# Performance work log

Measured on AMD Instinct MI355X. Metric: run time of the kernel, lower is better.

## Reference

```python
import jax, jax.numpy as jnp
import numpy as np

DIM = 2048
STATE = 16
BATCH = 2
SEQ = 2048
LN_EPS = 1e-5


def setup_inputs() -> dict:
    key = jax.random.key(0)
    ks = jax.random.split(key, 12)
    d, n = DIM, STATE
    inp = {
        "x": jax.random.normal(ks[0], (BATCH, SEQ, d), dtype=jnp.float32),
        "ln_gamma": jnp.ones((d,), dtype=jnp.float32),
        "ln_beta": jnp.zeros((d,), dtype=jnp.float32),
        # proj_in: Linear(d, 2d) (spectral-normed; weights treated as effective)
        "W_in": jax.random.normal(ks[1], (2 * d, d), dtype=jnp.float32) / np.sqrt(d),
        "b_in": jnp.zeros((2 * d,), dtype=jnp.float32),
        "state_A": jax.random.normal(ks[2], (n, d), dtype=jnp.float32) * 0.01,
        "W_B": jax.random.normal(ks[3], (n, d), dtype=jnp.float32) / np.sqrt(d),
        "b_B": jnp.zeros((n,), dtype=jnp.float32),
        "W_C": jax.random.normal(ks[4], (n, d), dtype=jnp.float32) / np.sqrt(d),
        "b_C": jnp.zeros((n,), dtype=jnp.float32),
        "W_dt": jax.random.normal(ks[5], (d, d), dtype=jnp.float32) / np.sqrt(d),
        "b_dt": jnp.zeros((d,), dtype=jnp.float32),
        "W_out": jax.random.normal(ks[6], (d, d), dtype=jnp.float32) / np.sqrt(d),
        "b_out": jnp.zeros((d,), dtype=jnp.float32),
    }
    return inp


def reference(x, ln_gamma, ln_beta, W_in, b_in, state_A, W_B, b_B, W_C, b_C,
              W_dt, b_dt, W_out, b_out):
    residual = x
    # LayerNorm over last dim
    mu = jnp.mean(x, axis=-1, keepdims=True)
    var = jnp.mean(jnp.square(x - mu), axis=-1, keepdims=True)
    xn = (x - mu) * jax.lax.rsqrt(var + LN_EPS) * ln_gamma + ln_beta
    # input projection and gate split
    xz = jnp.einsum('bsd,ed->bse', xn, W_in) + b_in          # (B,S,2D)
    x_ssm, z = jnp.split(xz, 2, axis=-1)                      # (B,S,D) each
    # dt = clamp(softplus(proj_dt(x_ssm)), max=1.0)
    dt = jnp.minimum(jax.nn.softplus(jnp.einsum('bsd,ed->bse', x_ssm, W_dt) + b_dt), 1.0)
    Bm = jnp.einsum('bsd,nd->bsn', x_ssm, W_B) + b_B          # (B,S,N)
    Cm = jnp.einsum('bsd,nd->bsn', x_ssm, W_C) + b_C          # (B,S,N)
    # A_bar[b,s,n,d] = exp(state_A[n,d] * dt[b,s,d])
    A_bar = jnp.exp(state_A[None, None, :, :] * dt[:, :, None, :])  # (B,S,N,D)
    # y[b,s,d] = sum_n C[b,s,n]*B[b,s,n]*A_bar[b,s,n,d] * x_ssm[b,s,d]
    y = jnp.einsum('bsn,bsnd->bsd', Cm * Bm, A_bar) * x_ssm
    gated = y * jax.nn.silu(z)
    out = jnp.einsum('bsd,ed->bse', gated, W_out) + b_out
    return out + residual
```

## Files before the change

### kernel.cpp

```cpp
#include <hip/hip_runtime.h>

typedef unsigned short u16;
typedef float f32x4 __attribute__((ext_vector_type(4)));
typedef __bf16 bf16x8 __attribute__((ext_vector_type(8)));

__device__ __forceinline__ u16 f2bf(float f) {
    unsigned u = __float_as_uint(f);
    u += 0x7FFFu + ((u >> 16) & 1u);
    return (u16)(u >> 16);
}
__device__ __forceinline__ float b2f(u16 h) {
    return __uint_as_float(((unsigned)h) << 16);
}

__device__ __forceinline__ void async16(const u16* g, u16* l) {
    __builtin_amdgcn_global_load_lds(
        (__attribute__((address_space(1))) void*)(u16*)g,
        (__attribute__((address_space(3))) void*)l,
        16, 0, 0);
}

#define T_TOK 4096
#define DIM   2048

__global__ __launch_bounds__(256) void castln_kernel(const float* __restrict__ W_in,
                                                     u16* __restrict__ wb_in,
                                                     const float* __restrict__ x,
                                                     const float* __restrict__ g,
                                                     const float* __restrict__ b,
                                                     u16* __restrict__ o) {
    __shared__ float s1[4], s2[4];
    int blk = blockIdx.x, tid = threadIdx.x;
    if (blk < 8192) {
        int i = blk * 256 + tid;
        float4 f = ((const float4*)W_in)[i];
        ushort4 u;
        u.x = f2bf(f.x); u.y = f2bf(f.y); u.z = f2bf(f.z); u.w = f2bf(f.w);
        ((ushort4*)wb_in)[i] = u;
        return;
    }
    int t = blk - 8192;
    int wave = tid >> 6, lane = tid & 63;
    size_t base = (size_t)t * DIM;
    int d0 = tid * 8;
    float4 v0 = *(const float4*)(x + base + d0);
    float4 v1 = *(const float4*)(x + base + d0 + 4);
    float v[8] = {v0.x, v0.y, v0.z, v0.w, v1.x, v1.y, v1.z, v1.w};
    float s = 0.f;
#pragma unroll
    for (int j = 0; j < 8; ++j) s += v[j];
#pragma unroll
    for (int o2 = 32; o2; o2 >>= 1) s += __shfl_xor(s, o2);
    if (lane == 0) s1[wave] = s;
    __syncthreads();
    float mu = (s1[0] + s1[1] + s1[2] + s1[3]) * (1.f / DIM);
    float q = 0.f;
#pragma unroll
    for (int j = 0; j < 8; ++j) { float dd = v[j] - mu; q += dd * dd; }
#pragma unroll
    for (int o2 = 32; o2; o2 >>= 1) q += __shfl_xor(q, o2);
    if (lane == 0) s2[wave] = q;
    __syncthreads();
    float var = (s2[0] + s2[1] + s2[2] + s2[3]) * (1.f / DIM);
    float rs = rsqrtf(var + 1e-5f);
    float4 g0 = *(const float4*)(g + d0), g1 = *(const float4*)(g + d0 + 4);
    float4 b0 = *(const float4*)(b + d0), b1 = *(const float4*)(b + d0 + 4);
    float gv[8] = {g0.x, g0.y, g0.z, g0.w, g1.x, g1.y, g1.z, g1.w};
    float bv[8] = {b0.x, b0.y, b0.z, b0.w, b1.x, b1.y, b1.z, b1.w};
    ushort4 r0, r1;
    u16* rp0 = (u16*)&r0; u16* rp1 = (u16*)&r1;
#pragma unroll
    for (int j = 0; j < 4; ++j) {
        rp0[j] = f2bf((v[j] - mu) * rs * gv[j] + bv[j]);
        rp1[j] = f2bf((v[j + 4] - mu) * rs * gv[j + 4] + bv[j + 4]);
    }
    *(ushort4*)(o + base + d0) = r0;
    *(ushort4*)(o + base + d0 + 4) = r1;
}

__global__ __launch_bounds__(256) void cast4_kernel(const float* __restrict__ s0, u16* __restrict__ d0, int n0,
                                                    const float* __restrict__ s1, u16* __restrict__ d1, int n1,
                                                    const float* __restrict__ s2, u16* __restrict__ d2, int n2,
                                                    const float* __restrict__ s3, u16* __restrict__ d3, int n3) {
    int j = blockIdx.x * 256 + threadIdx.x;
    const float* s; u16* d;
    if (j < n0) { s = s0; d = d0; }
    else {
        j -= n0;
        if (j < n1) { s = s1; d = d1; }
        else {
            j -= n1;
            if (j < n2) { s = s2; d = d2; }
            else { j -= n2; if (j >= n3) return; s = s3; d = d3; }
        }
    }
    float4 f = ((const float4*)s)[j];
    ushort4 u;
    u.x = f2bf(f.x); u.y = f2bf(f.y); u.z = f2bf(f.z); u.w = f2bf(f.w);
    ((ushort4*)d)[j] = u;
}

#define WBM 128
#define WBN 128
#define WBK 64

__global__ __launch_bounds__(256) void gemm_wide(const u16* __restrict__ A,
                                                 const u16* __restrict__ W,
                                                 const float* __restrict__ bias,
                                                 u16* __restrict__ Xs,
                                                 u16* __restrict__ Z, int K) {
    __shared__ __align__(16) u16 lAB[(WBM + WBN) * WBK];
    const int tid = threadIdx.x;
    const int wave = tid >> 6, lane = tid & 63;
    const int quad = lane >> 4, l16 = lane & 15;
    const int tM = blockIdx.x * WBM;
    const int tN = blockIdx.y * WBN;
    const int wr = wave >> 1, wc = wave & 1;

    const int rowin = tid >> 3;
    const int col8 = ((tid & 7) ^ (rowin & 7)) * 8;
    const u16* gptr[8];
    u16* ldst[8];
#pragma unroll
    for (int i = 0; i < 8; ++i) {
        int trow = i * 32 + rowin;
        const u16* src = (i < 4) ? (A + (size_t)(tM + trow) * 2048)
                                 : (W + (size_t)(tN + (trow - WBM)) * 2048);
        gptr[i] = src + col8;
        ldst[i] = &lAB[(i * 32 + wave * 8) * WBK];
    }

    int a_off[2][4], b_off[2][4];
#pragma unroll
    for (int h = 0; h < 2; ++h) {
#pragma unroll
        for (int mi = 0; mi < 4; ++mi)
            a_off[h][mi] = (wr * 64 + mi * 16 + l16) * WBK +
                           (((h * 4 + quad) ^ (l16 & 7)) * 8);
#pragma unroll
        for (int ni = 0; ni < 4; ++ni)
            b_off[h][ni] = (WBM + wc * 64 + ni * 16 + l16) * WBK +
                           (((h * 4 + quad) ^ (l16 & 7)) * 8);
    }

    f32x4 acc[4][4] = {};

    for (int kt = 0; kt < K; kt += WBK) {
#pragma unroll
        for (int i = 0; i < 8; ++i) async16(gptr[i] + kt, ldst[i]);
        __syncthreads();
#pragma unroll
        for (int h = 0; h < 2; ++h) {
            bf16x8 af[4], bfr[4];
#pragma unroll
            for (int i = 0; i < 4; ++i) af[i] = *(const bf16x8*)&lAB[a_off[h][i]];
#pragma unroll
            for (int i = 0; i < 4; ++i) bfr[i] = *(const bf16x8*)&lAB[b_off[h][i]];
#pragma unroll
            for (int mi = 0; mi < 4; ++mi)
#pragma unroll
                for (int ni = 0; ni < 4; ++ni)
                    acc[mi][ni] = __builtin_amdgcn_mfma_f32_16x16x32_bf16(
                        af[mi], bfr[ni], acc[mi][ni], 0, 0, 0);
        }
        __syncthreads();
    }

    const bool isb_z = (tN >= 2048);
    u16* dst = isb_z ? Z : Xs;
#pragma unroll
    for (int mi = 0; mi < 4; ++mi) {
#pragma unroll
        for (int ni = 0; ni < 4; ++ni) {
            int col = tN + wc * 64 + ni * 16 + l16;
            float bv = bias[col];
            int ocol = isb_z ? (col - 2048) : col;
#pragma unroll
            for (int r = 0; r < 4; ++r) {
                int row = tM + wr * 64 + mi * 16 + quad * 4 + r;
                dst[(size_t)row * 2048 + ocol] = f2bf(acc[mi][ni][r] + bv);
            }
        }
    }
}

#define NBM 128
#define NBN 64
#define NBK 64

template <int EPI>
__global__ __launch_bounds__(256) void gemm_nw(const u16* __restrict__ A, int lda,
                                               const u16* __restrict__ W, int ldw,
                                               const float* __restrict__ bias,
                                               const float* __restrict__ resid,
                                               void* __restrict__ C, int ldc, int K,
                                               u16* __restrict__ dots) {
    __shared__ __align__(16) u16 lAB[(NBM + NBN) * NBK];
    const int tid = threadIdx.x;
    const int wave = tid >> 6, lane = tid & 63;
    const int quad = lane >> 4, l16 = lane & 15;
    const int tM = blockIdx.x * NBM;
    const int tN = blockIdx.y * NBN;
    const int wr = wave >> 1, wc = wave & 1;

    const int rowin = tid >> 3;
    const int r3 = rowin & 7;
    const int col8 = ((tid & 7) ^ r3) * 8;
    const u16* gptr[6];
    u16* ldst[6];
#pragma unroll
    for (int i = 0; i < 6; ++i) {
        int trow = i * 32 + rowin;
        const u16* src = (i < 4) ? (A + (size_t)(tM + trow) * lda)
                                 : (W + (size_t)(tN + (trow - NBM)) * ldw);
        gptr[i] = src + col8;
        ldst[i] = &lAB[(i * 32 + wave * 8) * NBK];
    }

    int a_off[2][4], b_off[2][2];
#pragma unroll
    for (int h = 0; h < 2; ++h) {
#pragma unroll
        for (int mi = 0; mi < 4; ++mi)
            a_off[h][mi] = (wr * 64 + mi * 16 + l16) * NBK +
                           (((h * 4 + quad) ^ (l16 & 7)) * 8);
#pragma unroll
        for (int ni = 0; ni < 2; ++ni)
            b_off[h][ni] = (NBM + wc * 32 + ni * 16 + l16) * NBK +
                           (((h * 4 + quad) ^ (l16 & 7)) * 8);
    }

    f32x4 acc[4][2] = {};

    for (int kt = 0; kt < K; kt += NBK) {
#pragma unroll
        for (int i = 0; i < 6; ++i) async16(gptr[i] + kt, ldst[i]);
        __syncthreads();
        bf16x8 af[2][4], bfr[2][2];
#pragma unroll
        for (int h = 0; h < 2; ++h) {
#pragma unroll
            for (int mi = 0; mi < 4; ++mi) af[h][mi] = *(const bf16x8*)&lAB[a_off[h][mi]];
#pragma unroll
            for (int ni = 0; ni < 2; ++ni) bfr[h][ni] = *(const bf16x8*)&lAB[b_off[h][ni]];
        }
#pragma unroll
        for (int h = 0; h < 2; ++h)
#pragma unroll
            for (int mi = 0; mi < 4; ++mi)
#pragma unroll
                for (int ni = 0; ni < 2; ++ni)
                    acc[mi][ni] = __builtin_amdgcn_mfma_f32_16x16x32_bf16(
                        af[h][mi], bfr[h][ni], acc[mi][ni], 0, 0, 0);
        __syncthreads();
    }

#pragma unroll
    for (int mi = 0; mi < 4; ++mi) {
#pragma unroll
        for (int ni = 0; ni < 2; ++ni) {
            int col = tN + wc * 32 + ni * 16 + l16;
            float bv = (EPI == 1 && col >= 2048) ? 0.f : bias[col];
#pragma unroll
            for (int r = 0; r < 4; ++r) {
                int row = tM + wr * 64 + mi * 16 + quad * 4 + r;
                float v = acc[mi][ni][r] + bv;
                if constexpr (EPI == 1) {
                    if (col < 2048) {
                        float sp = (v > 20.f) ? v : log1pf(__expf(v));
                        ((u16*)C)[(size_t)row * ldc + col] = f2bf(fminf(sp, 1.0f));
                    } else if (col < 2080) {
                        dots[(size_t)row * 32 + (col - 2048)] = f2bf(v);
                    }
                } else {
                    size_t idx = (size_t)row * ldc + col;
                    ((float*)C)[idx] = v + resid[idx];
                }
            }
        }
    }
}

__global__ __launch_bounds__(256) void ssm_gate_kernel(const u16* __restrict__ dtb,
                                                       const u16* __restrict__ xsb,
                                                       const u16* __restrict__ zb,
                                                       const float* __restrict__ A,
                                                       const u16* __restrict__ dots,
                                                       const float* __restrict__ bB,
                                                       const float* __restrict__ bC,
                                                       u16* __restrict__ gated) {
    __shared__ float Pl[16];
    int t = blockIdx.x, tid = threadIdx.x;
    if (tid < 16) {
        float Bv = b2f(dots[(size_t)t * 32 + tid]) + bB[tid];
        float Cv = b2f(dots[(size_t)t * 32 + 16 + tid]) + bC[tid];
        Pl[tid] = Bv * Cv;
    }
    __syncthreads();
    size_t dbase = (size_t)t * DIM;
    int d0 = tid * 8;
    ushort4 dth[2], xsh[2], zh[2];
    dth[0] = *(const ushort4*)(dtb + dbase + d0);
    dth[1] = *(const ushort4*)(dtb + dbase + d0 + 4);
    xsh[0] = *(const ushort4*)(xsb + dbase + d0);
    xsh[1] = *(const ushort4*)(xsb + dbase + d0 + 4);
    zh[0]  = *(const ushort4*)(zb + dbase + d0);
    zh[1]  = *(const ushort4*)(zb + dbase + d0 + 4);
    float dtv[8], xsv[8], zv[8];
#pragma unroll
    for (int h = 0; h < 2; ++h) {
        const u16* dp = (const u16*)&dth[h];
        const u16* xp = (const u16*)&xsh[h];
        const u16* zp = (const u16*)&zh[h];
#pragma unroll
        for (int j = 0; j < 4; ++j) {
            dtv[h * 4 + j] = b2f(dp[j]);
            xsv[h * 4 + j] = b2f(xp[j]);
            zv[h * 4 + j]  = b2f(zp[j]);
        }
    }
    float s[8] = {};
#pragma unroll
    for (int n = 0; n < 16; ++n) {
        float4 a0 = *(const float4*)(A + n * DIM + d0);
        float4 a1 = *(const float4*)(A + n * DIM + d0 + 4);
        float pn = Pl[n];
        float av[8] = {a0.x, a0.y, a0.z, a0.w, a1.x, a1.y, a1.z, a1.w};
#pragma unroll
        for (int j = 0; j < 8; ++j) s[j] += pn * __expf(av[j] * dtv[j]);
    }
    ushort4 r0, r1;
    u16* rp0 = (u16*)&r0; u16* rp1 = (u16*)&r1;
#pragma unroll
    for (int j = 0; j < 8; ++j) {
        float y = s[j] * xsv[j];
        float sz = zv[j] * (1.0f / (1.0f + __expf(-zv[j])));
        u16 hv = f2bf(y * sz);
        if (j < 4) rp0[j] = hv; else rp1[j - 4] = hv;
    }
    *(ushort4*)(gated + dbase + d0) = r0;
    *(ushort4*)(gated + dbase + d0 + 4) = r1;
}

extern "C" void kernel_launch(void* const* d_in, const int* in_sizes, int n_in,
                              void* d_out, int out_size, void* d_ws, size_t ws_size,
                              hipStream_t stream) {
    const float* x      = (const float*)d_in[0];
    const float* ln_g   = (const float*)d_in[1];
    const float* ln_b   = (const float*)d_in[2];
    const float* W_in   = (const float*)d_in[3];
    const float* b_in   = (const float*)d_in[4];
    const float* stateA = (const float*)d_in[5];
    const float* W_B    = (const float*)d_in[6];
    const float* b_B    = (const float*)d_in[7];
    const float* W_C    = (const float*)d_in[8];
    const float* b_C    = (const float*)d_in[9];
    const float* W_dt   = (const float*)d_in[10];
    const float* b_dt   = (const float*)d_in[11];
    const float* W_out  = (const float*)d_in[12];
    const float* b_out  = (const float*)d_in[13];

    char* ws = (char*)d_ws;
    u16*   wb_in  = (u16*)(ws);
    u16*   wb_out = (u16*)(ws);
    u16*   xnb    = (u16*)(ws + 16777216);
    u16*   wb_dt  = (u16*)(ws + 16777216);
    u16*   gated  = (u16*)(ws + 16777216);
    u16*   xsb    = (u16*)(ws + 33554432);
    u16*   zb     = (u16*)(ws + 50331648);
    u16*   dtb    = (u16*)(ws + 67108864);
    u16*   dotsb  = (u16*)(ws + 83886080);

    castln_kernel<<<12288, 256, 0, stream>>>(W_in, wb_in, x, ln_g, ln_b, xnb);
    gemm_wide<<<dim3(32, 32), 256, 0, stream>>>(xnb, wb_in, b_in, xsb, zb, 2048);
    cast4_kernel<<<8256, 256, 0, stream>>>(
        W_dt, wb_dt, 1048576,
        W_B,  wb_dt + (size_t)2048 * 2048, 8192,
        W_C,  wb_dt + (size_t)2064 * 2048, 8192,
        W_out, wb_out, 1048576);
    gemm_nw<1><<<dim3(32, 33), 256, 0, stream>>>(xsb, 2048, wb_dt, 2048, b_dt,
                                                 nullptr, dtb, 2048, 2048, dotsb);
    ssm_gate_kernel<<<T_TOK, 256, 0, stream>>>(dtb, xsb, zb, stateA, dotsb,
                                               b_B, b_C, gated);
    gemm_nw<2><<<dim3(32, 32), 256, 0, stream>>>(gated, 2048, wb_out, 2048, b_out,
                                                 x, (float*)d_out, 2048, 2048, nullptr);
}
```

Baseline: 394.9 us.

## Use FP8 for dt projection and fold B/C projections into input GEMM

```diff
diff --git a/kernel.cpp b/kernel.cpp
--- a/kernel.cpp
+++ b/kernel.cpp
@@ -1,6 +1,8 @@
 #include <hip/hip_runtime.h>
 
 typedef unsigned short u16;
+typedef unsigned char u8;
+typedef unsigned int u32;
 typedef float f32x4 __attribute__((ext_vector_type(4)));
 typedef __bf16 bf16x8 __attribute__((ext_vector_type(8)));
 
@@ -13,9 +15,9 @@
     return __uint_as_float(((unsigned)h) << 16);
 }
 
-__device__ __forceinline__ void async16(const u16* g, u16* l) {
+__device__ __forceinline__ void async16(const void* g, void* l) {
     __builtin_amdgcn_global_load_lds(
-        (__attribute__((address_space(1))) void*)(u16*)g,
+        (__attribute__((address_space(1))) void*)g,
         (__attribute__((address_space(3))) void*)l,
         16, 0, 0);
 }
@@ -28,9 +30,16 @@
                                                      const float* __restrict__ x,
                                                      const float* __restrict__ g,
                                                      const float* __restrict__ b,
-                                                     u16* __restrict__ o) {
+                                                     u16* __restrict__ xnb,
+                                                     const float* __restrict__ W_B,
+                                                     const float* __restrict__ W_C,
+                                                     const float* __restrict__ b_in,
+                                                     const float* __restrict__ b_B,
+                                                     const float* __restrict__ b_C,
+                                                     float* __restrict__ be) {
     __shared__ float s1[4], s2[4];
     int blk = blockIdx.x, tid = threadIdx.x;
+    int wave = tid >> 6, lane = tid & 63;
     if (blk < 8192) {
         int i = blk * 256 + tid;
         float4 f = ((const float4*)W_in)[i];
@@ -39,65 +48,109 @@
         ((ushort4*)wb_in)[i] = u;
         return;
     }
-    int t = blk - 8192;
-    int wave = tid >> 6, lane = tid & 63;
-    size_t base = (size_t)t * DIM;
-    int d0 = tid * 8;
-    float4 v0 = *(const float4*)(x + base + d0);
-    float4 v1 = *(const float4*)(x + base + d0 + 4);
-    float v[8] = {v0.x, v0.y, v0.z, v0.w, v1.x, v1.y, v1.z, v1.w};
-    float s = 0.f;
-#pragma unroll
-    for (int j = 0; j < 8; ++j) s += v[j];
-#pragma unroll
-    for (int o2 = 32; o2; o2 >>= 1) s += __shfl_xor(s, o2);
-    if (lane == 0) s1[wave] = s;
-    __syncthreads();
-    float mu = (s1[0] + s1[1] + s1[2] + s1[3]) * (1.f / DIM);
-    float q = 0.f;
-#pragma unroll
-    for (int j = 0; j < 8; ++j) { float dd = v[j] - mu; q += dd * dd; }
-#pragma unroll
-    for (int o2 = 32; o2; o2 >>= 1) q += __shfl_xor(q, o2);
-    if (lane == 0) s2[wave] = q;
-    __syncthreads();
-    float var = (s2[0] + s2[1] + s2[2] + s2[3]) * (1.f / DIM);
-    float rs = rsqrtf(var + 1e-5f);
-    float4 g0 = *(const float4*)(g + d0), g1 = *(const float4*)(g + d0 + 4);
-    float4 b0 = *(const float4*)(b + d0), b1 = *(const float4*)(b + d0 + 4);
-    float gv[8] = {g0.x, g0.y, g0.z, g0.w, g1.x, g1.y, g1.z, g1.w};
-    float bv[8] = {b0.x, b0.y, b0.z, b0.w, b1.x, b1.y, b1.z, b1.w};
-    ushort4 r0, r1;
-    u16* rp0 = (u16*)&r0; u16* rp1 = (u16*)&r1;
-#pragma unroll
-    for (int j = 0; j < 4; ++j) {
-        rp0[j] = f2bf((v[j] - mu) * rs * gv[j] + bv[j]);
-        rp1[j] = f2bf((v[j + 4] - mu) * rs * gv[j + 4] + bv[j + 4]);
-    }
-    *(ushort4*)(o + base + d0) = r0;
-    *(ushort4*)(o + base + d0 + 4) = r1;
-}
-
-__global__ __launch_bounds__(256) void cast4_kernel(const float* __restrict__ s0, u16* __restrict__ d0, int n0,
-                                                    const float* __restrict__ s1, u16* __restrict__ d1, int n1,
-                                                    const float* __restrict__ s2, u16* __restrict__ d2, int n2,
-                                                    const float* __restrict__ s3, u16* __restrict__ d3, int n3) {
+    if (blk < 12288) {
+        int t = blk - 8192;
+        size_t base = (size_t)t * DIM;
+        int d0 = tid * 8;
+        float4 v0 = *(const float4*)(x + base + d0);
+        float4 v1 = *(const float4*)(x + base + d0 + 4);
+        float v[8] = {v0.x, v0.y, v0.z, v0.w, v1.x, v1.y, v1.z, v1.w};
+        float s = 0.f;
+#pragma unroll
+        for (int j = 0; j < 8; ++j) s += v[j];
+#pragma unroll
+        for (int o2 = 32; o2; o2 >>= 1) s += __shfl_xor(s, o2);
+        if (lane == 0) s1[wave] = s;
+        __syncthreads();
+        float mu = (s1[0] + s1[1] + s1[2] + s1[3]) * (1.f / DIM);
+        float q = 0.f;
+#pragma unroll
+        for (int j = 0; j < 8; ++j) { float dd = v[j] - mu; q += dd * dd; }
+#pragma unroll
+        for (int o2 = 32; o2; o2 >>= 1) q += __shfl_xor(q, o2);
+        if (lane == 0) s2[wave] = q;
+        __syncthreads();
+        float var = (s2[0] + s2[1] + s2[2] + s2[3]) * (1.f / DIM);
+        float rs = rsqrtf(var + 1e-5f);
+        float4 g0 = *(const float4*)(g + d0), g1 = *(const float4*)(g + d0 + 4);
+        float4 b0 = *(const float4*)(b + d0), b1 = *(const float4*)(b + d0 + 4);
+        float gv[8] = {g0.x, g0.y, g0.z, g0.w, g1.x, g1.y, g1.z, g1.w};
+        float bv[8] = {b0.x, b0.y, b0.z, b0.w, b1.x, b1.y, b1.z, b1.w};
+        ushort4 r0, r1;
+        u16* rp0 = (u16*)&r0; u16* rp1 = (u16*)&r1;
+#pragma unroll
+        for (int j = 0; j < 4; ++j) {
+            rp0[j] = f2bf((v[j] - mu) * rs * gv[j] + bv[j]);
+            rp1[j] = f2bf((v[j + 4] - mu) * rs * gv[j + 4] + bv[j + 4]);
+        }
+        *(ushort4*)(xnb + base + d0) = r0;
+        *(ushort4*)(xnb + base + d0 + 4) = r1;
+        return;
+    }
+    int cb = blk - 12288;
+    if (cb < 32) {
+        int e = cb * 64 + lane;
+        const float* wrow[8];
+#pragma unroll
+        for (int i = 0; i < 8; ++i) {
+            int n = wave * 8 + i;
+            wrow[i] = (n < 16) ? (W_B + (size_t)n * DIM) : (W_C + (size_t)(n - 16) * DIM);
+        }
+        float acc[8] = {};
+        for (int d = 0; d < DIM; ++d) {
+            float wv = W_in[(size_t)d * DIM + e];
+#pragma unroll
+            for (int i = 0; i < 8; ++i) acc[i] += wrow[i][d] * wv;
+        }
+#pragma unroll
+        for (int i = 0; i < 8; ++i)
+            wb_in[(size_t)(4096 + wave * 8 + i) * DIM + e] = f2bf(acc[i]);
+        return;
+    }
+    int n = tid >> 3, sl = tid & 7;
+    if (n < 32) {
+        const float* wrow = (n < 16) ? (W_B + (size_t)n * DIM)
+                                     : (W_C + (size_t)(n - 16) * DIM);
+        float a = 0.f;
+        for (int d = sl; d < DIM; d += 8) a += wrow[d] * b_in[d];
+        a += __shfl_xor(a, 1); a += __shfl_xor(a, 2); a += __shfl_xor(a, 4);
+        if (sl == 0) be[n] = a + ((n < 16) ? b_B[n] : b_C[n - 16]);
+    }
+}
+
+__global__ __launch_bounds__(256) void cast8_kernel(const float* __restrict__ W_dt,
+                                                    u8* __restrict__ w8,
+                                                    const u16* __restrict__ xsb,
+                                                    u8* __restrict__ xs8,
+                                                    const float* __restrict__ W_out,
+                                                    u16* __restrict__ wb_out) {
     int j = blockIdx.x * 256 + threadIdx.x;
-    const float* s; u16* d;
-    if (j < n0) { s = s0; d = d0; }
-    else {
-        j -= n0;
-        if (j < n1) { s = s1; d = d1; }
-        else {
-            j -= n1;
-            if (j < n2) { s = s2; d = d2; }
-            else { j -= n2; if (j >= n3) return; s = s3; d = d3; }
-        }
-    }
-    float4 f = ((const float4*)s)[j];
-    ushort4 u;
-    u.x = f2bf(f.x); u.y = f2bf(f.y); u.z = f2bf(f.z); u.w = f2bf(f.w);
-    ((ushort4*)d)[j] = u;
+    if (j < 1048576) {
+        float4 f = ((const float4*)W_dt)[j];
+        int p = __builtin_amdgcn_cvt_pk_fp8_f32(f.x, f.y, 0, false);
+        p = __builtin_amdgcn_cvt_pk_fp8_f32(f.z, f.w, p, true);
+        ((u32*)w8)[j] = p;
+        return;
+    }
+    j -= 1048576;
+    if (j < 1048576) {
+        ushort4 h0 = ((const ushort4*)xsb)[2 * j];
+        ushort4 h1 = ((const ushort4*)xsb)[2 * j + 1];
+        int p0 = __builtin_amdgcn_cvt_pk_fp8_f32(b2f(h0.x), b2f(h0.y), 0, false);
+        p0 = __builtin_amdgcn_cvt_pk_fp8_f32(b2f(h0.z), b2f(h0.w), p0, true);
+        int p1 = __builtin_amdgcn_cvt_pk_fp8_f32(b2f(h1.x), b2f(h1.y), 0, false);
+        p1 = __builtin_amdgcn_cvt_pk_fp8_f32(b2f(h1.z), b2f(h1.w), p1, true);
+        ((u32*)xs8)[2 * j] = p0;
+        ((u32*)xs8)[2 * j + 1] = p1;
+        return;
+    }
+    j -= 1048576;
+    if (j < 1048576) {
+        float4 f = ((const float4*)W_out)[j];
+        ushort4 u;
+        u.x = f2bf(f.x); u.y = f2bf(f.y); u.z = f2bf(f.z); u.w = f2bf(f.w);
+        ((ushort4*)wb_out)[j] = u;
+    }
 }
 
 #define WBM 128
@@ -108,7 +161,8 @@
                                                  const u16* __restrict__ W,
                                                  const float* __restrict__ bias,
                                                  u16* __restrict__ Xs,
-                                                 u16* __restrict__ Z, int K) {
+                                                 u16* __restrict__ Z,
+                                                 u16* __restrict__ dots, int K) {
     __shared__ __align__(16) u16 lAB[(WBM + WBN) * WBK];
     const int tid = threadIdx.x;
     const int wave = tid >> 6, lane = tid & 63;
@@ -166,6 +220,22 @@
         __syncthreads();
     }
 
+    if (tN >= 4096) {
+        if (wc == 0) {
+#pragma unroll
+            for (int mi = 0; mi < 4; ++mi)
+#pragma unroll
+                for (int ni = 0; ni < 2; ++ni) {
+                    int nc = ni * 16 + l16;
+#pragma unroll
+                    for (int r = 0; r < 4; ++r) {
+                        int row = tM + wr * 64 + mi * 16 + quad * 4 + r;
+                        dots[(size_t)row * 32 + nc] = f2bf(acc[mi][ni][r]);
+                    }
+                }
+        }
+        return;
+    }
     const bool isb_z = (tN >= 2048);
     u16* dst = isb_z ? Z : Xs;
 #pragma unroll
@@ -184,37 +254,114 @@
     }
 }
 
-#define NBM 128
-#define NBN 64
-#define NBK 64
-
-template <int EPI>
-__global__ __launch_bounds__(256) void gemm_nw(const u16* __restrict__ A, int lda,
-                                               const u16* __restrict__ W, int ldw,
-                                               const float* __restrict__ bias,
-                                               const float* __restrict__ resid,
-                                               void* __restrict__ C, int ldc, int K,
-                                               u16* __restrict__ dots) {
-    __shared__ __align__(16) u16 lAB[(NBM + NBN) * NBK];
+__global__ __launch_bounds__(256) void gemm_dt8(const u8* __restrict__ A,
+                                                const u8* __restrict__ W,
+                                                const float* __restrict__ bias,
+                                                u8* __restrict__ dt8) {
+    __shared__ __align__(16) u8 lAB[192 * 128];
     const int tid = threadIdx.x;
     const int wave = tid >> 6, lane = tid & 63;
     const int quad = lane >> 4, l16 = lane & 15;
-    const int tM = blockIdx.x * NBM;
-    const int tN = blockIdx.y * NBN;
+    const int tM = blockIdx.x * 128;
+    const int tN = blockIdx.y * 64;
     const int wr = wave >> 1, wc = wave & 1;
 
     const int rowin = tid >> 3;
-    const int r3 = rowin & 7;
-    const int col8 = ((tid & 7) ^ r3) * 8;
+    const int col16 = ((tid & 7) ^ (rowin & 7)) * 16;
+    const u8* gptr[6];
+    u8* ldst[6];
+#pragma unroll
+    for (int i = 0; i < 6; ++i) {
+        int trow = i * 32 + rowin;
+        const u8* src = (i < 4) ? (A + (size_t)(tM + trow) * 2048)
+                                : (W + (size_t)(tN + (trow - 128)) * 2048);
+        gptr[i] = src + col16;
+        ldst[i] = &lAB[(i * 32 + wave * 8) * 128];
+    }
+
+    int a_off[4][4], b_off[4][2];
+#pragma unroll
+    for (int h = 0; h < 4; ++h) {
+        int c = 2 * h + (quad >> 1);
+        int half = (quad & 1) * 8;
+#pragma unroll
+        for (int mi = 0; mi < 4; ++mi) {
+            int row = wr * 64 + mi * 16 + l16;
+            a_off[h][mi] = row * 128 + ((c ^ (row & 7)) << 4) + half;
+        }
+#pragma unroll
+        for (int ni = 0; ni < 2; ++ni) {
+            int row = 128 + wc * 32 + ni * 16 + l16;
+            b_off[h][ni] = row * 128 + ((c ^ (row & 7)) << 4) + half;
+        }
+    }
+
+    f32x4 acc[4][2] = {};
+
+    for (int kt = 0; kt < 2048; kt += 128) {
+#pragma unroll
+        for (int i = 0; i < 6; ++i) async16(gptr[i] + kt, ldst[i]);
+        __syncthreads();
+#pragma unroll
+        for (int h = 0; h < 4; ++h) {
+            long long af[4], bf[2];
+#pragma unroll
+            for (int mi = 0; mi < 4; ++mi) af[mi] = *(const long long*)&lAB[a_off[h][mi]];
+#pragma unroll
+            for (int ni = 0; ni < 2; ++ni) bf[ni] = *(const long long*)&lAB[b_off[h][ni]];
+#pragma unroll
+            for (int mi = 0; mi < 4; ++mi)
+#pragma unroll
+                for (int ni = 0; ni < 2; ++ni)
+                    acc[mi][ni] = __builtin_amdgcn_mfma_f32_16x16x32_fp8_fp8(
+                        af[mi], bf[ni], acc[mi][ni], 0, 0, 0);
+        }
+        __syncthreads();
+    }
+
+#pragma unroll
+    for (int mi = 0; mi < 4; ++mi) {
+#pragma unroll
+        for (int ni = 0; ni < 2; ++ni) {
+            int col = tN + wc * 32 + ni * 16 + l16;
+            float bv = bias[col];
+#pragma unroll
+            for (int r = 0; r < 4; ++r) {
+                int row = tM + wr * 64 + mi * 16 + quad * 4 + r;
+                float v = acc[mi][ni][r] + bv;
+                float sp = (v > 20.f) ? v : log1pf(__expf(v));
+                sp = fminf(sp, 1.0f);
+                int p = __builtin_amdgcn_cvt_pk_fp8_f32(sp, sp, 0, false);
+                dt8[(size_t)row * 2048 + col] = (u8)(p & 0xFF);
+            }
+        }
+    }
+}
+
+__global__ __launch_bounds__(256) void gemm_out(const u16* __restrict__ A,
+                                                const u16* __restrict__ W,
+                                                const float* __restrict__ bias,
+                                                const float* __restrict__ resid,
+                                                float* __restrict__ C) {
+    __shared__ __align__(16) u16 lAB[192 * 64];
+    const int tid = threadIdx.x;
+    const int wave = tid >> 6, lane = tid & 63;
+    const int quad = lane >> 4, l16 = lane & 15;
+    const int tM = blockIdx.x * 128;
+    const int tN = blockIdx.y * 64;
+    const int wr = wave >> 1, wc = wave & 1;
+
+    const int rowin = tid >> 3;
+    const int col8 = ((tid & 7) ^ (rowin & 7)) * 8;
     const u16* gptr[6];
     u16* ldst[6];
 #pragma unroll
     for (int i = 0; i < 6; ++i) {
         int trow = i * 32 + rowin;
-        const u16* src = (i < 4) ? (A + (size_t)(tM + trow) * lda)
-                                 : (W + (size_t)(tN + (trow - NBM)) * ldw);
+        const u16* src = (i < 4) ? (A + (size_t)(tM + trow) * 2048)
+                                 : (W + (size_t)(tN + (trow - 128)) * 2048);
         gptr[i] = src + col8;
-        ldst[i] = &lAB[(i * 32 + wave * 8) * NBK];
+        ldst[i] = &lAB[(i * 32 + wave * 8) * 64];
     }
 
     int a_off[2][4], b_off[2][2];
@@ -222,17 +369,17 @@
     for (int h = 0; h < 2; ++h) {
 #pragma unroll
         for (int mi = 0; mi < 4; ++mi)
-            a_off[h][mi] = (wr * 64 + mi * 16 + l16) * NBK +
+            a_off[h][mi] = (wr * 64 + mi * 16 + l16) * 64 +
                            (((h * 4 + quad) ^ (l16 & 7)) * 8);
 #pragma unroll
         for (int ni = 0; ni < 2; ++ni)
-            b_off[h][ni] = (NBM + wc * 32 + ni * 16 + l16) * NBK +
+            b_off[h][ni] = (128 + wc * 32 + ni * 16 + l16) * 64 +
                            (((h * 4 + quad) ^ (l16 & 7)) * 8);
     }
 
     f32x4 acc[4][2] = {};
 
-    for (int kt = 0; kt < K; kt += NBK) {
+    for (int kt = 0; kt < 2048; kt += 64) {
 #pragma unroll
         for (int i = 0; i < 6; ++i) async16(gptr[i] + kt, ldst[i]);
         __syncthreads();
@@ -260,61 +407,56 @@
 #pragma unroll
         for (int ni = 0; ni < 2; ++ni) {
             int col = tN + wc * 32 + ni * 16 + l16;
-            float bv = (EPI == 1 && col >= 2048) ? 0.f : bias[col];
+            float bv = bias[col];
 #pragma unroll
             for (int r = 0; r < 4; ++r) {
                 int row = tM + wr * 64 + mi * 16 + quad * 4 + r;
-                float v = acc[mi][ni][r] + bv;
-                if constexpr (EPI == 1) {
-                    if (col < 2048) {
-                        float sp = (v > 20.f) ? v : log1pf(__expf(v));
-                        ((u16*)C)[(size_t)row * ldc + col] = f2bf(fminf(sp, 1.0f));
-                    } else if (col < 2080) {
-                        dots[(size_t)row * 32 + (col - 2048)] = f2bf(v);
-                    }
-                } else {
-                    size_t idx = (size_t)row * ldc + col;
-                    ((float*)C)[idx] = v + resid[idx];
-                }
+                size_t idx = (size_t)row * 2048 + col;
+                C[idx] = acc[mi][ni][r] + bv + resid[idx];
             }
         }
     }
 }
 
-__global__ __launch_bounds__(256) void ssm_gate_kernel(const u16* __restrict__ dtb,
+__global__ __launch_bounds__(256) void ssm_gate_kernel(const u8* __restrict__ dt8,
                                                        const u16* __restrict__ xsb,
                                                        const u16* __restrict__ zb,
                                                        const float* __restrict__ A,
                                                        const u16* __restrict__ dots,
-                                                       const float* __restrict__ bB,
-                                                       const float* __restrict__ bC,
+                                                       const float* __restrict__ be,
                                                        u16* __restrict__ gated) {
     __shared__ float Pl[16];
     int t = blockIdx.x, tid = threadIdx.x;
     if (tid < 16) {
-        float Bv = b2f(dots[(size_t)t * 32 + tid]) + bB[tid];
-        float Cv = b2f(dots[(size_t)t * 32 + 16 + tid]) + bC[tid];
+        float Bv = b2f(dots[(size_t)t * 32 + tid]) + be[tid];
+        float Cv = b2f(dots[(size_t)t * 32 + 16 + tid]) + be[16 + tid];
         Pl[tid] = Bv * Cv;
     }
     __syncthreads();
     size_t dbase = (size_t)t * DIM;
     int d0 = tid * 8;
-    ushort4 dth[2], xsh[2], zh[2];
-    dth[0] = *(const ushort4*)(dtb + dbase + d0);
-    dth[1] = *(const ushort4*)(dtb + dbase + d0 + 4);
+    unsigned long long dl = *(const unsigned long long*)(dt8 + dbase + d0);
+    unsigned dlo = (unsigned)dl, dhi = (unsigned)(dl >> 32);
+    ushort4 xsh[2], zh[2];
     xsh[0] = *(const ushort4*)(xsb + dbase + d0);
     xsh[1] = *(const ushort4*)(xsb + dbase + d0 + 4);
     zh[0]  = *(const ushort4*)(zb + dbase + d0);
     zh[1]  = *(const ushort4*)(zb + dbase + d0 + 4);
     float dtv[8], xsv[8], zv[8];
+    dtv[0] = __builtin_amdgcn_cvt_f32_fp8(dlo, 0);
+    dtv[1] = __builtin_amdgcn_cvt_f32_fp8(dlo, 1);
+    dtv[2] = __builtin_amdgcn_cvt_f32_fp8(dlo, 2);
+    dtv[3] = __builtin_amdgcn_cvt_f32_fp8(dlo, 3);
+    dtv[4] = __builtin_amdgcn_cvt_f32_fp8(dhi, 0);
+    dtv[5] = __builtin_amdgcn_cvt_f32_fp8(dhi, 1);
+    dtv[6] = __builtin_amdgcn_cvt_f32_fp8(dhi, 2);
+    dtv[7] = __builtin_amdgcn_cvt_f32_fp8(dhi, 3);
 #pragma unroll
     for (int h = 0; h < 2; ++h) {
-        const u16* dp = (const u16*)&dth[h];
         const u16* xp = (const u16*)&xsh[h];
         const u16* zp = (const u16*)&zh[h];
 #pragma unroll
         for (int j = 0; j < 4; ++j) {
-            dtv[h * 4 + j] = b2f(dp[j]);
             xsv[h * 4 + j] = b2f(xp[j]);
             zv[h * 4 + j]  = b2f(zp[j]);
         }
@@ -362,26 +504,25 @@
 
     char* ws = (char*)d_ws;
     u16*   wb_in  = (u16*)(ws);
-    u16*   wb_out = (u16*)(ws);
-    u16*   xnb    = (u16*)(ws + 16777216);
-    u16*   wb_dt  = (u16*)(ws + 16777216);
-    u16*   gated  = (u16*)(ws + 16777216);
-    u16*   xsb    = (u16*)(ws + 33554432);
-    u16*   zb     = (u16*)(ws + 50331648);
-    u16*   dtb    = (u16*)(ws + 67108864);
-    u16*   dotsb  = (u16*)(ws + 83886080);
-
-    castln_kernel<<<12288, 256, 0, stream>>>(W_in, wb_in, x, ln_g, ln_b, xnb);
-    gemm_wide<<<dim3(32, 32), 256, 0, stream>>>(xnb, wb_in, b_in, xsb, zb, 2048);
-    cast4_kernel<<<8256, 256, 0, stream>>>(
-        W_dt, wb_dt, 1048576,
-        W_B,  wb_dt + (size_t)2048 * 2048, 8192,
-        W_C,  wb_dt + (size_t)2064 * 2048, 8192,
-        W_out, wb_out, 1048576);
-    gemm_nw<1><<<dim3(32, 33), 256, 0, stream>>>(xsb, 2048, wb_dt, 2048, b_dt,
-                                                 nullptr, dtb, 2048, 2048, dotsb);
-    ssm_gate_kernel<<<T_TOK, 256, 0, stream>>>(dtb, xsb, zb, stateA, dotsb,
-                                               b_B, b_C, gated);
-    gemm_nw<2><<<dim3(32, 32), 256, 0, stream>>>(gated, 2048, wb_out, 2048, b_out,
-                                                 x, (float*)d_out, 2048, 2048, nullptr);
-}
+    u8*    w8_dt  = (u8*)(ws);
+    u16*   gated  = (u16*)(ws);
+    u16*   xnb    = (u16*)(ws + 16908288);
+    u16*   wb_out = (u16*)(ws + 16908288);
+    u8*    xs8    = (u8*)(ws + 16908288 + 8388608);
+    u16*   xsb    = (u16*)(ws + 33685504);
+    u16*   zb     = (u16*)(ws + 50462720);
+    u8*    dt8    = (u8*)(ws + 67239936);
+    u16*   dotsb  = (u16*)(ws + 75628544);
+    float* be     = (float*)(ws + 75890688);
+
+    castln_kernel<<<12321, 256, 0, stream>>>(W_in, wb_in, x, ln_g, ln_b, xnb,
+                                             W_B, W_C, b_in, b_B, b_C, be);
+    gemm_wide<<<dim3(32, 33), 256, 0, stream>>>(xnb, wb_in, b_in, xsb, zb,
+                                                dotsb, 2048);
+    cast8_kernel<<<12288, 256, 0, stream>>>(W_dt, w8_dt, xsb, xs8, W_out, wb_out);
+    gemm_dt8<<<dim3(32, 32), 256, 0, stream>>>(xs8, w8_dt, b_dt, dt8);
+    ssm_gate_kernel<<<T_TOK, 256, 0, stream>>>(dt8, xsb, zb, stateA, dotsb,
+                                               be, gated);
+    gemm_out<<<dim3(32, 32), 256, 0, stream>>>(gated, wb_out, b_out, x,
+                                               (float*)d_out);
+}
```

New measurement: 623.6 us. 57.9% more time.
